# Optimization experiments

Measured on AMD Instinct MI355X. Metric: run time of the kernel, lower is better.

## Reference

```python
import jax, jax.numpy as jnp
import numpy as np
import math

B, N, D, L = 2, 256, 128, 4
TD = D // 2  # time embed dim
GROUPS = 32

def _interleave_sincos(v):
    # torch: stack((v[...,0::2].sin(), v[...,1::2].cos()), -1).flatten(last two)
    s = jnp.sin(v[..., 0::2])
    c = jnp.cos(v[..., 1::2])
    return jnp.stack([s, c], axis=-1).reshape(v.shape[:-1] + (-1,))

def _pos_embed(coords):
    # PositionEmbeddingSine(num_pos_feats=D//2, normalize=True, scale=2*pi)
    npf = D // 2
    dim_t = jnp.power(10000.0, 2.0 * jnp.floor(jnp.arange(npf, dtype=jnp.float32) / 2.0) / npf)
    scale = 2.0 * math.pi
    py = _interleave_sincos((coords[:, :, 0] * scale)[:, :, None] / dim_t)
    px = _interleave_sincos((coords[:, :, 1] * scale)[:, :, None] / dim_t)
    return jnp.concatenate([py, px], axis=-1)  # (B,N,D)

def _edge_pos_embed(adj):
    # ScalarEmbeddingSine(num_pos_feats=D, normalize=False)
    dim_t = jnp.power(10000.0, 2.0 * jnp.floor(jnp.arange(D, dtype=jnp.float32) / 2.0) / D)
    return _interleave_sincos(adj[:, :, :, None] / dim_t)  # (B,N,N,D)

def _timestep_embedding(t, dim):
    half = dim // 2
    freqs = jnp.exp(-math.log(10000.0) * jnp.arange(half, dtype=jnp.float32) / half)
    args = t.astype(jnp.float32)[:, None] * freqs
    return jnp.concatenate([jnp.cos(args), jnp.sin(args)], axis=-1)  # (B,D)

def _ln(x, s, b, eps=1e-5):
    mu = jnp.mean(x, -1, keepdims=True)
    var = jnp.var(x, -1, keepdims=True)
    return (x - mu) * jax.lax.rsqrt(var + eps) * s + b

def _gn(x, s, b, groups=GROUPS, eps=1e-5):
    # GroupNorm32 over (B, C, H, W)
    bb, c, h, w = x.shape
    xg = x.reshape(bb, groups, c // groups, h, w)
    mu = jnp.mean(xg, (2, 3, 4), keepdims=True)
    var = jnp.var(xg, (2, 3, 4), keepdims=True)
    xg = (xg - mu) * jax.lax.rsqrt(var + eps)
    return xg.reshape(bb, c, h, w) * s[None, :, None, None] + b[None, :, None, None]

def _forward(coords, adj_t, t, node_W, node_b, edge_W, edge_b, te1_W, te1_b, te2_W, te2_b,
             A_W, A_b, B_W, B_b, C_W, C_b, U_W, U_b, V_W, V_b,
             lnh_s, lnh_b, lne_s, lne_b, tl_W, tl_b,
             plo_ln_s, plo_ln_b, plo_W, plo_b, gn_s, gn_b, conv_W, conv_b):
    x = _pos_embed(coords) @ node_W + node_b            # (B,N,D)
    e = _edge_pos_embed(adj_t) @ edge_W + edge_b        # (B,N,N,D)
    te = _timestep_embedding(t, D) @ te1_W + te1_b
    te = jax.nn.relu(te) @ te2_W + te2_b                # (B,TD)
    for i in range(L):
        x_in, e_in = x, e
        # GatedGCNLayer (mode=direct, no internal residual)
        Uh = x @ U_W[i] + U_b[i]
        Vh = x @ V_W[i] + V_b[i]
        gate_input = ((x @ A_W[i] + A_b[i])[:, :, None, :]
                      + (x @ B_W[i] + B_b[i])[:, None, :, :]
                      + (e @ C_W[i] + C_b[i]))          # (B,N,N,D)
        gates = jax.nn.sigmoid(gate_input)
        agg = jnp.einsum('bijd,bjd->bid', gates, Vh)     # sum over neighbors j
        h_new = jax.nn.relu(_ln(Uh + agg, lnh_s[i], lnh_b[i]))
        e_new = jax.nn.relu(_ln(gate_input, lne_s[i], lne_b[i]))
        # time injection into edges: ReLU -> Linear(TD->D)
        e_new = e_new + (jax.nn.relu(te) @ tl_W[i] + tl_b[i])[:, None, None, :]
        # external residuals + per-layer out (LN -> SiLU -> Linear)
        x = x_in + h_new
        e = e_in + jax.nn.silu(_ln(e_new, plo_ln_s[i], plo_ln_b[i])) @ plo_W[i] + plo_b[i]
    eo = jnp.transpose(e, (0, 3, 1, 2))                  # (B,D,N,N)
    eo = jax.nn.relu(_gn(eo, gn_s, gn_b))
    out = jnp.einsum('bdij,do->boij', eo, conv_W) + conv_b[None, :, None, None]
    return out                                           # (B,1,N,N)

def setup_inputs() -> dict:
    key = jax.random.key(0)
    ks = iter(jax.random.split(key, 64))
    def w(shape, scale=0.02):
        return jax.random.normal(next(ks), shape, dtype=jnp.float32) * scale
    f32 = jnp.float32
    return {
        'coords': jax.random.uniform(next(ks), (B, N, 2), dtype=f32),
        'adj_t': jax.random.normal(next(ks), (B, N, N), dtype=f32),
        't': jax.random.uniform(next(ks), (B,), dtype=f32) * 1000.0,
        'node_W': w((D, D)), 'node_b': jnp.zeros((D,), f32),
        'edge_W': w((D, D)), 'edge_b': jnp.zeros((D,), f32),
        'te1_W': w((D, TD)), 'te1_b': jnp.zeros((TD,), f32),
        'te2_W': w((TD, TD)), 'te2_b': jnp.zeros((TD,), f32),
        'A_W': w((L, D, D)), 'A_b': jnp.zeros((L, D), f32),
        'B_W': w((L, D, D)), 'B_b': jnp.zeros((L, D), f32),
        'C_W': w((L, D, D)), 'C_b': jnp.zeros((L, D), f32),
        'U_W': w((L, D, D)), 'U_b': jnp.zeros((L, D), f32),
        'V_W': w((L, D, D)), 'V_b': jnp.zeros((L, D), f32),
        'lnh_s': jnp.ones((L, D), f32), 'lnh_b': jnp.zeros((L, D), f32),
        'lne_s': jnp.ones((L, D), f32), 'lne_b': jnp.zeros((L, D), f32),
        'tl_W': w((L, TD, D)), 'tl_b': jnp.zeros((L, D), f32),
        'plo_ln_s': jnp.ones((L, D), f32), 'plo_ln_b': jnp.zeros((L, D), f32),
        'plo_W': w((L, D, D)), 'plo_b': jnp.zeros((L, D), f32),
        'gn_s': jnp.ones((D,), f32), 'gn_b': jnp.zeros((D,), f32),
        'conv_W': w((D, 1)), 'conv_b': jnp.zeros((1,), f32),
    }

def reference(coords, adj_t, t, node_W, node_b, edge_W, edge_b, te1_W, te1_b, te2_W, te2_b,
              A_W, A_b, B_W, B_b, C_W, C_b, U_W, U_b, V_W, V_b,
              lnh_s, lnh_b, lne_s, lne_b, tl_W, tl_b,
              plo_ln_s, plo_ln_b, plo_W, plo_b, gn_s, gn_b, conv_W, conv_b):
    return _forward(coords, adj_t, t, node_W, node_b, edge_W, edge_b, te1_W, te1_b, te2_W, te2_b,
                    A_W, A_b, B_W, B_b, C_W, C_b, U_W, U_b, V_W, V_b,
                    lnh_s, lnh_b, lne_s, lne_b, tl_W, tl_b,
                    plo_ln_s, plo_ln_b, plo_W, plo_b, gn_s, gn_b, conv_W, conv_b)
```

## Files before the change

### kernel.cpp

```cpp
#include <hip/hip_runtime.h>
#include <hip/hip_bf16.h>

typedef unsigned short u16;
typedef __attribute__((ext_vector_type(8))) short short8;
typedef __attribute__((ext_vector_type(8))) unsigned short ushort8;
typedef __attribute__((ext_vector_type(4))) float f32x4;

#define BB 2
#define NN 256
#define DD 128
#define TDD 64
#define LL 4
#define NGROUP 32
#define NROWS (BB*NN*NN)
#define LDS_STR 68

#define LOG1E4 9.210340371976184f
#define TWO_PI 6.283185307179586f

#define TILE_GEMM(AT, WPTR, ACC) do {                                          \
  _Pragma("unroll 4")                                                          \
  for (int k = 0; k < 128; ++k) {                                              \
    const float4 w4 = *reinterpret_cast<const float4*>((WPTR) + k*128 + tx*4); \
    const float4 a0 = *reinterpret_cast<const float4*>(&(AT)[k*LDS_STR + ty*8]);     \
    const float4 a1 = *reinterpret_cast<const float4*>(&(AT)[k*LDS_STR + ty*8 + 4]); \
    const float av[8] = {a0.x,a0.y,a0.z,a0.w,a1.x,a1.y,a1.z,a1.w};             \
    const float wv[4] = {w4.x,w4.y,w4.z,w4.w};                                 \
    _Pragma("unroll") for (int r = 0; r < 8; ++r)                              \
      _Pragma("unroll") for (int c = 0; c < 4; ++c)                            \
        ACC[r][c] += av[r]*wv[c];                                              \
  }                                                                            \
} while (0)

__device__ __forceinline__ float sigmoidf_(float x) {
  return 1.f / (1.f + __expf(-x));
}

__device__ __forceinline__ u16 f2bf(float f) {
  union { float f; unsigned int u; } c; c.f = f;
  unsigned int r = (c.u + 0x7FFFu + ((c.u >> 16) & 1u)) >> 16;
  return (u16)r;
}

__global__ __launch_bounds__(512) void k_time(
    const float* __restrict__ t,
    const float* __restrict__ te1_W, const float* __restrict__ te1_b,
    const float* __restrict__ te2_W, const float* __restrict__ te2_b,
    const float* __restrict__ tl_W,  const float* __restrict__ tl_b,
    float* __restrict__ tproj) {
  __shared__ float temb[BB][128], h1[BB][64], rt[BB][64];
  const int tid = threadIdx.x;
  const int b  = tid >> 8;
  const int t2 = tid & 255;
  const float tv = t[b];
  if (t2 < 128) {
    int j = t2 & 63;
    float f = expf(-LOG1E4 * (float)j / 64.f);
    float a = tv * f;
    temb[b][t2] = (t2 < 64) ? cosf(a) : sinf(a);
  }
  __syncthreads();
  if (t2 < 64) {
    float acc = te1_b[t2];
#pragma unroll
    for (int k = 0; k < 128; ++k) acc += temb[b][k] * te1_W[k*64 + t2];
    h1[b][t2] = fmaxf(acc, 0.f);
  }
  __syncthreads();
  if (t2 < 64) {
    float acc = te2_b[t2];
#pragma unroll
    for (int k = 0; k < 64; ++k) acc += h1[b][k] * te2_W[k*64 + t2];
    rt[b][t2] = fmaxf(acc, 0.f);
  }
  __syncthreads();
  if (t2 < 128) {
#pragma unroll
    for (int i = 0; i < LL; ++i) {
      float acc = tl_b[i*128 + t2];
#pragma unroll
      for (int k = 0; k < 64; ++k) acc += rt[b][k] * tl_W[(i*64 + k)*128 + t2];
      tproj[(i*BB + b)*128 + t2] = acc;
    }
  }
}

__global__ __launch_bounds__(256) void k_node_embed(
    const float* __restrict__ coords, const float* __restrict__ W,
    const float* __restrict__ bias, float* __restrict__ x_out) {
  __shared__ float at[128*LDS_STR];
  int tid = threadIdx.x;
  int row = tid >> 2, part = tid & 3;
  int R = blockIdx.x*64 + row;
  float cy = coords[R*2 + 0], cx = coords[R*2 + 1];
#pragma unroll
  for (int q = 0; q < 32; ++q) {
    int c = part*32 + q;
    int k = (c < 64) ? c : c - 64;
    float v = (c < 64) ? cy : cx;
    int m = k >> 1;
    float inv = __expf(-LOG1E4 * (float)m / 32.f);
    float a = v * TWO_PI * inv;
    at[c*LDS_STR + row] = (k & 1) ? __cosf(a) : __sinf(a);
  }
  __syncthreads();
  int tx = tid & 31, ty = tid >> 5;
  float acc[8][4] = {};
  TILE_GEMM(at, W, acc);
  float4 bb4 = *reinterpret_cast<const float4*>(bias + tx*4);
#pragma unroll
  for (int r = 0; r < 8; ++r) {
    int R2 = blockIdx.x*64 + ty*8 + r;
    float4 o = {acc[r][0]+bb4.x, acc[r][1]+bb4.y, acc[r][2]+bb4.z, acc[r][3]+bb4.w};
    *reinterpret_cast<float4*>(x_out + (size_t)R2*128 + tx*4) = o;
  }
}

__global__ __launch_bounds__(256) void k_wprep_e(
    const float* __restrict__ EW, u16* __restrict__ WTE) {
  int idx = blockIdx.x*256 + threadIdx.x;
  int n = idx >> 7, k = idx & 127;
  WTE[n*128 + k] = f2bf(EW[(size_t)k*128 + n]);
}

__global__ __launch_bounds__(256, 3) void k_edge_embed2(
    const float* __restrict__ adj, const u16* __restrict__ WTE,
    const float* __restrict__ bias, float* __restrict__ e_out) {
  __shared__ __align__(16) u16 Abuf[64*128];
  __shared__ __align__(16) u16 Wbuf[128*128];

  const int tid = threadIdx.x;
  const int blk = blockIdx.x;
  const int w  = tid >> 6;
  const int l  = tid & 63;
  const int lg = l >> 4;
  const int ln = l & 15;

  {
    const int r = tid >> 1, h = tid & 1;
    const int r7 = r & 7;
    const u16* src = WTE + r*128;
    u16* dst = Wbuf + r*128;
#pragma unroll
    for (int q = 0; q < 8; ++q) {
      int c = h*8 + q;
      short8 v = *reinterpret_cast<const short8*>(src + c*8);
      *reinterpret_cast<short8*>(dst + ((c ^ r7) << 3)) = v;
    }
  }
  {
    const int r = tid >> 2;
    const int p = tid & 3;
    const float v = adj[(size_t)blk*64 + r];
    const int r7 = r & 7;
    u16* arow = Abuf + r*128;
#pragma unroll
    for (int q = 0; q < 4; ++q) {
      u16 h8[8];
#pragma unroll
      for (int j = 0; j < 8; ++j) {
        int k = (p*4 + q)*8 + j;
        int m = k >> 1;
        float inv = __expf(-LOG1E4 * (float)m / 64.f);
        float a = v * inv;
        h8[j] = f2bf((k & 1) ? __cosf(a) : __sinf(a));
      }
      int pc = (p*4 + q) ^ r7;
      *reinterpret_cast<ushort8*>(arow + pc*8) = *reinterpret_cast<ushort8*>(h8);
    }
  }
  __syncthreads();

  f32x4 acc[8];
#pragma unroll
  for (int nt = 0; nt < 8; ++nt) {
    const float bv = bias[nt*16 + ln];
#pragma unroll
    for (int rg = 0; rg < 4; ++rg) acc[nt][rg] = bv;
  }
  {
    const u16* arow = Abuf + (w*16 + ln)*128;
    const int r7 = ln & 7;
#pragma unroll
    for (int ks = 0; ks < 4; ++ks) {
      short8 a = *reinterpret_cast<const short8*>(arow + (((ks*4 + lg) ^ r7) << 3));
#pragma unroll
      for (int nt = 0; nt < 8; ++nt) {
        short8 bw = *reinterpret_cast<const short8*>(
            Wbuf + (nt*16 + ln)*128 + (((ks*4 + lg) ^ (ln & 7)) << 3));
        acc[nt] = __builtin_amdgcn_mfma_f32_16x16x32_bf16(a, bw, acc[nt], 0, 0, 0);
      }
    }
  }
#pragma unroll
  for (int nt = 0; nt < 8; ++nt)
#pragma unroll
    for (int rg = 0; rg < 4; ++rg)
      e_out[((size_t)blk*64 + w*16 + lg*4 + rg)*128 + nt*16 + ln] = acc[nt][rg];
}

__global__ __launch_bounds__(128) void k_node4(
    const float* __restrict__ x,
    const float* __restrict__ UW, const float* __restrict__ Ub,
    const float* __restrict__ VW, const float* __restrict__ Vb,
    const float* __restrict__ AW, const float* __restrict__ Ab,
    const float* __restrict__ BW, const float* __restrict__ Bb,
    float* __restrict__ Uh, float* __restrict__ Vh,
    float* __restrict__ Axo, float* __restrict__ Bxo) {
  __shared__ float xr[128];
  int R = blockIdx.x, d = threadIdx.x;
  xr[d] = x[(size_t)R*128 + d];
  __syncthreads();
  float au = Ub[d], av = Vb[d], aa = Ab[d], ab = Bb[d];
  for (int k = 0; k < 128; ++k) {
    float xv = xr[k];
    au += xv * UW[k*128 + d];
    av += xv * VW[k*128 + d];
    aa += xv * AW[k*128 + d];
    ab += xv * BW[k*128 + d];
  }
  Uh[(size_t)R*128 + d] = au;
  Vh[(size_t)R*128 + d] = av;
  Axo[(size_t)R*128 + d] = aa;
  Bxo[(size_t)R*128 + d] = ab;
}

__global__ __launch_bounds__(128) void k_xnode(
    const float* __restrict__ aggP,
    const float* __restrict__ lnh_s, const float* __restrict__ lnh_b,
    float* __restrict__ x,
    const float* __restrict__ UW, const float* __restrict__ Ub,
    const float* __restrict__ VW, const float* __restrict__ Vb,
    const float* __restrict__ AW, const float* __restrict__ Ab,
    const float* __restrict__ BW, const float* __restrict__ Bb,
    float* __restrict__ Uh, float* __restrict__ Vh,
    float* __restrict__ Axo, float* __restrict__ Bxo) {
  __shared__ float xr[128];
  __shared__ float red[4];
  int bi = blockIdx.x, d = threadIdx.x;
  float u = Uh[(size_t)bi*128 + d];
#pragma unroll
  for (int st = 0; st < 16; ++st) u += aggP[((size_t)bi*16 + st)*128 + d];
  float s = u, s2 = u*u;
#pragma unroll
  for (int m = 1; m <= 32; m <<= 1) { s += __shfl_xor(s, m); s2 += __shfl_xor(s2, m); }
  int wid = d >> 6;
  if ((d & 63) == 0) { red[wid] = s; red[2 + wid] = s2; }
  __syncthreads();
  s = red[0] + red[1];  s2 = red[2] + red[3];
  float mean = s * (1.f/128.f);
  float rs = rsqrtf(s2 * (1.f/128.f) - mean*mean + 1e-5f);
  float xv = x[(size_t)bi*128 + d] + fmaxf((u - mean)*rs*lnh_s[d] + lnh_b[d], 0.f);
  x[(size_t)bi*128 + d] = xv;
  xr[d] = xv;
  __syncthreads();
  float au = Ub[d], av = Vb[d], aa = Ab[d], ab = Bb[d];
  for (int k = 0; k < 128; ++k) {
    float xk = xr[k];
    au += xk * UW[k*128 + d];
    av += xk * VW[k*128 + d];
    aa += xk * AW[k*128 + d];
    ab += xk * BW[k*128 + d];
  }
  Uh[(size_t)bi*128 + d] = au;
  Vh[(size_t)bi*128 + d] = av;
  Axo[(size_t)bi*128 + d] = aa;
  Bxo[(size_t)bi*128 + d] = ab;
}

__global__ __launch_bounds__(256) void k_wprep(
    const float* __restrict__ CW, const float* __restrict__ PW,
    u16* __restrict__ WTC, u16* __restrict__ WTP) {
  int idx = blockIdx.x*256 + threadIdx.x;
  int m = idx >> 14;
  int r = idx & 16383;
  int layer = m >> 1;
  int n = r >> 7, k = r & 127;
  if ((m & 1) == 0)
    WTC[layer*16384 + n*128 + k] = f2bf(CW[(size_t)layer*16384 + k*128 + n]);
  else
    WTP[layer*16384 + n*128 + k] = f2bf(PW[(size_t)layer*16384 + k*128 + n]);
}

__global__ __launch_bounds__(512, 2) void k_layer(
    float* __restrict__ e,
    const u16* __restrict__ WTC, const u16* __restrict__ WTP,
    const float* __restrict__ Cb, const float* __restrict__ Ax,
    const float* __restrict__ Bx, const float* __restrict__ Vh,
    const float* __restrict__ lnes_g, const float* __restrict__ lneb_g,
    const float* __restrict__ tp_g,
    const float* __restrict__ plos_g, const float* __restrict__ plobl_g,
    const float* __restrict__ plob_g,
    float* __restrict__ aggP) {

  __shared__ __align__(16) u16 Abuf[128*128];
  __shared__ __align__(16) u16 Wbuf[128*128];

  const int tid = threadIdx.x;
  const int blk0 = blockIdx.x;
  const int blk = ((blk0 & 7) << 7) | (blk0 >> 3);
  const int bi  = blk >> 1;
  const int b   = bi >> 8;
  const int jh  = blk & 1;
  const size_t rbase = (size_t)bi*256 + jh*128;

  const int w  = tid >> 6;
  const int l  = tid & 63;
  const int lg = l >> 4;
  const int ln = l & 15;

  {
    const int r = tid >> 2;
    const int p = tid & 3;
    const float* src = e + (rbase + r)*128 + p*32;
    const int r7 = r & 7;
    u16* arow = Abuf + r*128;
#pragma unroll
    for (int q = 0; q < 4; ++q) {
      float4 f0 = *reinterpret_cast<const float4*>(src + q*8);
      float4 f1 = *reinterpret_cast<const float4*>(src + q*8 + 4);
      int pc = (p*4 + q) ^ r7;
      ushort8 h = {f2bf(f0.x),f2bf(f0.y),f2bf(f0.z),f2bf(f0.w),
                   f2bf(f1.x),f2bf(f1.y),f2bf(f1.z),f2bf(f1.w)};
      *reinterpret_cast<ushort8*>(arow + pc*8) = h;
    }
  }
  {
    const int r = tid >> 2;
    const int h = tid & 3;
    const int r7 = r & 7;
    const u16* src = WTC + r*128;
    u16* dst = Wbuf + r*128;
#pragma unroll
    for (int q = 0; q < 4; ++q) {
      int c = h*4 + q;
      short8 v = *reinterpret_cast<const short8*>(src + c*8);
      *reinterpret_cast<short8*>(dst + ((c ^ r7) << 3)) = v;
    }
  }
  __syncthreads();

  const int lrow0 = w*16 + lg*4;
  const int jrow0 = jh*128 + lrow0;

  f32x4 acc[8];
#pragma unroll
  for (int nt = 0; nt < 8; ++nt) {
    const int c = nt*16 + ln;
    const float cbax = Cb[c] + Ax[(size_t)bi*128 + c];
#pragma unroll
    for (int rg = 0; rg < 4; ++rg)
      acc[nt][rg] = cbax + Bx[((size_t)b*256 + jrow0 + rg)*128 + c];
  }

  {
    const u16* arow = Abuf + (w*16 + ln)*128;
    const int r7 = ln & 7;
#pragma unroll
    for (int ks = 0; ks < 4; ++ks) {
      short8 a = *reinterpret_cast<const short8*>(arow + (((ks*4 + lg) ^ r7) << 3));
#pragma unroll
      for (int nt = 0; nt < 8; ++nt) {
        short8 bw = *reinterpret_cast<const short8*>(
            Wbuf + (nt*16 + ln)*128 + (((ks*4 + lg) ^ (ln & 7)) << 3));
        acc[nt] = __builtin_amdgcn_mfma_f32_16x16x32_bf16(a, bw, acc[nt], 0, 0, 0);
      }
    }
  }

  float av[8] = {0.f,0.f,0.f,0.f,0.f,0.f,0.f,0.f};
  float tp_[8], ls_[8], lb_[8], ps_[8], pl_[8];
#pragma unroll
  for (int nt = 0; nt < 8; ++nt) {
    const int c = nt*16 + ln;
    tp_[nt] = tp_g[b*128 + c];
    ls_[nt] = lnes_g[c];  lb_[nt] = lneb_g[c];
    ps_[nt] = plos_g[c];  pl_[nt] = plobl_g[c];
  }

#pragma unroll
  for (int rg = 0; rg < 4; ++rg) {
    float ss = 0.f, s2 = 0.f;
#pragma unroll
    for (int nt = 0; nt < 8; ++nt) { float g = acc[nt][rg]; ss += g; s2 += g*g; }
    ss += __shfl_xor(ss, 1);  s2 += __shfl_xor(s2, 1);
    ss += __shfl_xor(ss, 2);  s2 += __shfl_xor(s2, 2);
    ss += __shfl_xor(ss, 4);  s2 += __shfl_xor(s2, 4);
    ss += __shfl_xor(ss, 8);  s2 += __shfl_xor(s2, 8);
    const float mean = ss * (1.f/128.f);
    const float rs = rsqrtf(s2 * (1.f/128.f) - mean*mean + 1e-5f);
    const size_t vrow = ((size_t)b*256 + jrow0 + rg)*128;
    float s3 = 0.f, s4 = 0.f;
#pragma unroll
    for (int nt = 0; nt < 8; ++nt) {
      const float g = acc[nt][rg];
      av[nt] += Vh[vrow + nt*16 + ln] * sigmoidf_(g);
      float tv = fmaxf((g - mean)*rs*ls_[nt] + lb_[nt], 0.f) + tp_[nt];
      acc[nt][rg] = tv;
      s3 += tv;  s4 += tv*tv;
    }
    s3 += __shfl_xor(s3, 1);  s4 += __shfl_xor(s4, 1);
    s3 += __shfl_xor(s3, 2);  s4 += __shfl_xor(s4, 2);
    s3 += __shfl_xor(s3, 4);  s4 += __shfl_xor(s4, 4);
    s3 += __shfl_xor(s3, 8);  s4 += __shfl_xor(s4, 8);
    const float mean2 = s3 * (1.f/128.f);
    const float rs2 = rsqrtf(s4 * (1.f/128.f) - mean2*mean2 + 1e-5f);
    const int rr = lrow0 + rg;
    const int rr7 = rr & 7;
#pragma unroll
    for (int nt = 0; nt < 8; ++nt) {
      float vv = (acc[nt][rg] - mean2)*rs2*ps_[nt] + pl_[nt];
      vv = vv * sigmoidf_(vv);
      const int cc = nt*16 + ln;
      const int pc = (cc >> 3) ^ rr7;
      Abuf[rr*128 + pc*8 + (cc & 7)] = f2bf(vv);
    }
  }

  __syncthreads();
  {
    const int r = tid >> 2;
    const int h = tid & 3;
    const int r7 = r & 7;
    const u16* src = WTP + r*128;
    u16* dst = Wbuf + r*128;
#pragma unroll
    for (int q = 0; q < 4; ++q) {
      int c = h*4 + q;
      short8 v = *reinterpret_cast<const short8*>(src + c*8);
      *reinterpret_cast<short8*>(dst + ((c ^ r7) << 3)) = v;
    }
  }
  __syncthreads();

  f32x4 acc2[8];
#pragma unroll
  for (int nt = 0; nt < 8; ++nt) acc2[nt] = (f32x4)(0.f);
  {
    const u16* arow = Abuf + (w*16 + ln)*128;
    const int r7 = ln & 7;
#pragma unroll
    for (int ks = 0; ks < 4; ++ks) {
      short8 a = *reinterpret_cast<const short8*>(arow + (((ks*4 + lg) ^ r7) << 3));
#pragma unroll
      for (int nt = 0; nt < 8; ++nt) {
        short8 bw = *reinterpret_cast<const short8*>(
            Wbuf + (nt*16 + ln)*128 + (((ks*4 + lg) ^ (ln & 7)) << 3));
        acc2[nt] = __builtin_amdgcn_mfma_f32_16x16x32_bf16(a, bw, acc2[nt], 0, 0, 0);
      }
    }
  }

#pragma unroll
  for (int nt = 0; nt < 8; ++nt) {
    const float pbv = plob_g[nt*16 + ln];
#pragma unroll
    for (int rg = 0; rg < 4; ++rg) {
      float* ep = e + (rbase + lrow0 + rg)*128 + nt*16 + ln;
      *ep = *ep + acc2[nt][rg] + pbv;
    }
  }

#pragma unroll
  for (int nt = 0; nt < 8; ++nt) {
    float v = av[nt];
    v += __shfl_xor(v, 16);
    v += __shfl_xor(v, 32);
    av[nt] = v;
  }
  if (lg == 0) {
#pragma unroll
    for (int nt = 0; nt < 8; ++nt)
      aggP[((size_t)blk*8 + w)*128 + nt*16 + ln] = av[nt];
  }
}

__global__ __launch_bounds__(128) void k_xupd(
    const float* __restrict__ aggP, const float* __restrict__ Uh,
    const float* __restrict__ lnh_s, const float* __restrict__ lnh_b,
    float* __restrict__ x) {
  int bi = blockIdx.x, d = threadIdx.x;
  float u = Uh[(size_t)bi*128 + d];
#pragma unroll
  for (int st = 0; st < 16; ++st) u += aggP[((size_t)bi*16 + st)*128 + d];
  float s = u, s2 = u*u;
#pragma unroll
  for (int m = 1; m <= 32; m <<= 1) { s += __shfl_xor(s, m); s2 += __shfl_xor(s2, m); }
  __shared__ float red[4];
  int wid = d >> 6;
  if ((d & 63) == 0) { red[wid] = s; red[2 + wid] = s2; }
  __syncthreads();
  s = red[0] + red[1];  s2 = red[2] + red[3];
  float mean = s * (1.f/128.f);
  float rs = rsqrtf(s2 * (1.f/128.f) - mean*mean + 1e-5f);
  x[(size_t)bi*128 + d] += fmaxf((u - mean)*rs*lnh_s[d] + lnh_b[d], 0.f);
}

__global__ __launch_bounds__(128) void k_zero(float* __restrict__ p) {
  p[threadIdx.x] = 0.f;
}

__global__ __launch_bounds__(256) void k_gnstats2(
    const float* __restrict__ e, float* __restrict__ sraw) {
  const int blk = blockIdx.x;
  const int b = blk >> 8;
  const int c = threadIdx.x & 31;
  const int r0 = threadIdx.x >> 5;
  float s = 0.f, s2 = 0.f;
  for (int it = 0; it < 32; ++it) {
    size_t row = (size_t)blk*256 + it*8 + r0;
    float4 f = *reinterpret_cast<const float4*>(e + row*128 + c*4);
    s  += f.x + f.y + f.z + f.w;
    s2 += f.x*f.x + f.y*f.y + f.z*f.z + f.w*f.w;
  }
  __shared__ float red[256], red2[256];
  red[threadIdx.x] = s;  red2[threadIdx.x] = s2;
  __syncthreads();
  if (threadIdx.x < 32) {
    float S = 0.f, S2 = 0.f;
#pragma unroll
    for (int k = 0; k < 8; ++k) { S += red[k*32 + threadIdx.x]; S2 += red2[k*32 + threadIdx.x]; }
    atomicAdd(&sraw[((size_t)b*32 + threadIdx.x)*2],     S);
    atomicAdd(&sraw[((size_t)b*32 + threadIdx.x)*2 + 1], S2);
  }
}

__global__ __launch_bounds__(64) void k_gnfin(
    const float* __restrict__ raw, float* __restrict__ stats) {
  int i = threadIdx.x;
  const float cnt = (float)(NN*NN*4);
  float S  = raw[i*2];
  float S2 = raw[i*2 + 1];
  float mean = S / cnt;
  float var = S2 / cnt - mean*mean;
  stats[i*2]     = mean;
  stats[i*2 + 1] = rsqrtf(var + 1e-5f);
}

__global__ __launch_bounds__(256) void k_out(
    const float* __restrict__ e, const float* __restrict__ stats,
    const float* __restrict__ gn_s, const float* __restrict__ gn_b,
    const float* __restrict__ convW, const float* __restrict__ convb,
    float* __restrict__ out) {
  int tid = threadIdx.x;
  int row = tid >> 2, part = tid & 3;
  size_t R = (size_t)blockIdx.x*64 + row;
  size_t b = R >> 16;
  float acc = 0.f;
  const float4* er = reinterpret_cast<const float4*>(e + R*128 + part*32);
#pragma unroll
  for (int q = 0; q < 8; ++q) {
    float4 f = er[q];
    float fv[4] = {f.x, f.y, f.z, f.w};
#pragma unroll
    for (int lidx = 0; lidx < 4; ++lidx) {
      int c = part*32 + q*4 + lidx;
      int g = c >> 2;
      float mean = stats[(b*NGROUP + g)*2 + 0];
      float rs   = stats[(b*NGROUP + g)*2 + 1];
      float t = (fv[lidx] - mean)*rs*gn_s[c] + gn_b[c];
      acc += fmaxf(t, 0.f) * convW[c];
    }
  }
  acc += __shfl_xor(acc, 1);
  acc += __shfl_xor(acc, 2);
  if (part == 0) out[R] = acc + convb[0];
}

extern "C" void kernel_launch(void* const* d_in, const int* in_sizes, int n_in,
                              void* d_out, int out_size, void* d_ws, size_t ws_size,
                              hipStream_t stream) {
  const float* coords  = (const float*)d_in[0];
  const float* adj_t   = (const float*)d_in[1];
  const float* t       = (const float*)d_in[2];
  const float* node_W  = (const float*)d_in[3];
  const float* node_b  = (const float*)d_in[4];
  const float* edge_W  = (const float*)d_in[5];
  const float* edge_b  = (const float*)d_in[6];
  const float* te1_W   = (const float*)d_in[7];
  const float* te1_b   = (const float*)d_in[8];
  const float* te2_W   = (const float*)d_in[9];
  const float* te2_b   = (const float*)d_in[10];
  const float* A_W     = (const float*)d_in[11];
  const float* A_b     = (const float*)d_in[12];
  const float* B_W     = (const float*)d_in[13];
  const float* B_b     = (const float*)d_in[14];
  const float* C_W     = (const float*)d_in[15];
  const float* C_b     = (const float*)d_in[16];
  const float* U_W     = (const float*)d_in[17];
  const float* U_b     = (const float*)d_in[18];
  const float* V_W     = (const float*)d_in[19];
  const float* V_b     = (const float*)d_in[20];
  const float* lnh_s   = (const float*)d_in[21];
  const float* lnh_b   = (const float*)d_in[22];
  const float* lne_s   = (const float*)d_in[23];
  const float* lne_b   = (const float*)d_in[24];
  const float* tl_W    = (const float*)d_in[25];
  const float* tl_b    = (const float*)d_in[26];
  const float* plo_ln_s= (const float*)d_in[27];
  const float* plo_ln_b= (const float*)d_in[28];
  const float* plo_W   = (const float*)d_in[29];
  const float* plo_b   = (const float*)d_in[30];
  const float* gn_s    = (const float*)d_in[31];
  const float* gn_b    = (const float*)d_in[32];
  const float* conv_W  = (const float*)d_in[33];
  const float* conv_b  = (const float*)d_in[34];

  float* ws    = (float*)d_ws;
  float* e     = ws;
  float* x     = e + (size_t)NROWS*128;
  float* Uh    = x + 65536;
  float* Vh    = Uh + 65536;
  float* Ax    = Vh + 65536;
  float* Bx    = Ax + 65536;
  float* tproj = Bx + 65536;
  float* sraw  = tproj + 1024;
  float* stats = sraw + 128;
  float* aggP  = stats + 128;
  u16*   WTC   = (u16*)(aggP + 1048576);
  u16*   WTP   = WTC + (size_t)LL*16384;
  u16*   WTE   = WTP + (size_t)LL*16384;

  k_zero<<<1, 128, 0, stream>>>(sraw);
  k_wprep<<<512, 256, 0, stream>>>(C_W, plo_W, WTC, WTP);
  k_wprep_e<<<64, 256, 0, stream>>>(edge_W, WTE);
  k_time<<<1, 512, 0, stream>>>(t, te1_W, te1_b, te2_W, te2_b, tl_W, tl_b, tproj);
  k_node_embed<<<8, 256, 0, stream>>>(coords, node_W, node_b, x);
  k_edge_embed2<<<NROWS/64, 256, 0, stream>>>(adj_t, WTE, edge_b, e);

  for (int i = 0; i < LL; ++i) {
    if (i == 0) {
      k_node4<<<BB*NN, 128, 0, stream>>>(x,
          U_W, U_b, V_W, V_b, A_W, A_b, B_W, B_b,
          Uh, Vh, Ax, Bx);
    } else {
      k_xnode<<<BB*NN, 128, 0, stream>>>(aggP,
          lnh_s + (i-1)*128, lnh_b + (i-1)*128, x,
          U_W + (size_t)i*16384, U_b + i*128,
          V_W + (size_t)i*16384, V_b + i*128,
          A_W + (size_t)i*16384, A_b + i*128,
          B_W + (size_t)i*16384, B_b + i*128,
          Uh, Vh, Ax, Bx);
    }
    k_layer<<<NROWS/128, 512, 0, stream>>>(e,
        WTC + (size_t)i*16384, WTP + (size_t)i*16384,
        C_b + i*128, Ax, Bx, Vh,
        lne_s + i*128, lne_b + i*128,
        tproj + i*BB*128,
        plo_ln_s + i*128, plo_ln_b + i*128, plo_b + i*128,
        aggP);
  }
  k_xupd<<<BB*NN, 128, 0, stream>>>(aggP, Uh, lnh_s + 3*128, lnh_b + 3*128, x);

  k_gnstats2<<<512, 256, 0, stream>>>(e, sraw);
  k_gnfin<<<1, 64, 0, stream>>>(sraw, stats);
  k_out<<<NROWS/64, 256, 0, stream>>>(e, stats, gn_s, gn_b, conv_W, conv_b,
                                      (float*)d_out);
}
```

Before: 411.2 us.

## Fuse GroupNorm statistics into last edge layer and finalize stats in output kernel

Adds a variant of the edge layer kernel, used for the last layer only, that accumulates per-group sum and sum-of-squares of the updated edge features into shared memory and then atomically into a global buffer. This removes a separate full pass over the edge tensor (k_gnstats2) and the k_gnfin launch. k_out now computes mean and rstd per block from the raw sums into shared memory. The fused kernel adds shared and global atomics and extra register pressure in the last layer.

```diff
diff --git a/kernel.cpp b/kernel.cpp
--- a/kernel.cpp
+++ b/kernel.cpp
@@ -475,6 +475,222 @@
   }
 }
 
+__global__ __launch_bounds__(512, 2) void k_layer_s(
+    float* __restrict__ e,
+    const u16* __restrict__ WTC, const u16* __restrict__ WTP,
+    const float* __restrict__ Cb, const float* __restrict__ Ax,
+    const float* __restrict__ Bx, const float* __restrict__ Vh,
+    const float* __restrict__ lnes_g, const float* __restrict__ lneb_g,
+    const float* __restrict__ tp_g,
+    const float* __restrict__ plos_g, const float* __restrict__ plobl_g,
+    const float* __restrict__ plob_g,
+    float* __restrict__ aggP, float* __restrict__ sraw) {
+
+  __shared__ __align__(16) u16 Abuf[128*128];
+  __shared__ __align__(16) u16 Wbuf[128*128];
+  __shared__ float sgrp[64];
+
+  const int tid = threadIdx.x;
+  const int blk0 = blockIdx.x;
+  const int blk = ((blk0 & 7) << 7) | (blk0 >> 3);
+  const int bi  = blk >> 1;
+  const int b   = bi >> 8;
+  const int jh  = blk & 1;
+  const size_t rbase = (size_t)bi*256 + jh*128;
+
+  const int w  = tid >> 6;
+  const int l  = tid & 63;
+  const int lg = l >> 4;
+  const int ln = l & 15;
+
+  {
+    const int r = tid >> 2;
+    const int p = tid & 3;
+    const float* src = e + (rbase + r)*128 + p*32;
+    const int r7 = r & 7;
+    u16* arow = Abuf + r*128;
+#pragma unroll
+    for (int q = 0; q < 4; ++q) {
+      float4 f0 = *reinterpret_cast<const float4*>(src + q*8);
+      float4 f1 = *reinterpret_cast<const float4*>(src + q*8 + 4);
+      int pc = (p*4 + q) ^ r7;
+      ushort8 h = {f2bf(f0.x),f2bf(f0.y),f2bf(f0.z),f2bf(f0.w),
+                   f2bf(f1.x),f2bf(f1.y),f2bf(f1.z),f2bf(f1.w)};
+      *reinterpret_cast<ushort8*>(arow + pc*8) = h;
+    }
+  }
+  {
+    const int r = tid >> 2;
+    const int h = tid & 3;
+    const int r7 = r & 7;
+    const u16* src = WTC + r*128;
+    u16* dst = Wbuf + r*128;
+#pragma unroll
+    for (int q = 0; q < 4; ++q) {
+      int c = h*4 + q;
+      short8 v = *reinterpret_cast<const short8*>(src + c*8);
+      *reinterpret_cast<short8*>(dst + ((c ^ r7) << 3)) = v;
+    }
+  }
+  if (tid < 64) sgrp[tid] = 0.f;
+  __syncthreads();
+
+  const int lrow0 = w*16 + lg*4;
+  const int jrow0 = jh*128 + lrow0;
+
+  f32x4 acc[8];
+#pragma unroll
+  for (int nt = 0; nt < 8; ++nt) {
+    const int c = nt*16 + ln;
+    const float cbax = Cb[c] + Ax[(size_t)bi*128 + c];
+#pragma unroll
+    for (int rg = 0; rg < 4; ++rg)
+      acc[nt][rg] = cbax + Bx[((size_t)b*256 + jrow0 + rg)*128 + c];
+  }
+
+  {
+    const u16* arow = Abuf + (w*16 + ln)*128;
+    const int r7 = ln & 7;
+#pragma unroll
+    for (int ks = 0; ks < 4; ++ks) {
+      short8 a = *reinterpret_cast<const short8*>(arow + (((ks*4 + lg) ^ r7) << 3));
+#pragma unroll
+      for (int nt = 0; nt < 8; ++nt) {
+        short8 bw = *reinterpret_cast<const short8*>(
+            Wbuf + (nt*16 + ln)*128 + (((ks*4 + lg) ^ (ln & 7)) << 3));
+        acc[nt] = __builtin_amdgcn_mfma_f32_16x16x32_bf16(a, bw, acc[nt], 0, 0, 0);
+      }
+    }
+  }
+
+  float av[8] = {0.f,0.f,0.f,0.f,0.f,0.f,0.f,0.f};
+  float tp_[8], ls_[8], lb_[8], ps_[8], pl_[8];
+#pragma unroll
+  for (int nt = 0; nt < 8; ++nt) {
+    const int c = nt*16 + ln;
+    tp_[nt] = tp_g[b*128 + c];
+    ls_[nt] = lnes_g[c];  lb_[nt] = lneb_g[c];
+    ps_[nt] = plos_g[c];  pl_[nt] = plobl_g[c];
+  }
+
+#pragma unroll
+  for (int rg = 0; rg < 4; ++rg) {
+    float ss = 0.f, s2 = 0.f;
+#pragma unroll
+    for (int nt = 0; nt < 8; ++nt) { float g = acc[nt][rg]; ss += g; s2 += g*g; }
+    ss += __shfl_xor(ss, 1);  s2 += __shfl_xor(s2, 1);
+    ss += __shfl_xor(ss, 2);  s2 += __shfl_xor(s2, 2);
+    ss += __shfl_xor(ss, 4);  s2 += __shfl_xor(s2, 4);
+    ss += __shfl_xor(ss, 8);  s2 += __shfl_xor(s2, 8);
+    const float mean = ss * (1.f/128.f);
+    const float rs = rsqrtf(s2 * (1.f/128.f) - mean*mean + 1e-5f);
+    const size_t vrow = ((size_t)b*256 + jrow0 + rg)*128;
+    float s3 = 0.f, s4 = 0.f;
+#pragma unroll
+    for (int nt = 0; nt < 8; ++nt) {
+      const float g = acc[nt][rg];
+      av[nt] += Vh[vrow + nt*16 + ln] * sigmoidf_(g);
+      float tv = fmaxf((g - mean)*rs*ls_[nt] + lb_[nt], 0.f) + tp_[nt];
+      acc[nt][rg] = tv;
+      s3 += tv;  s4 += tv*tv;
+    }
+    s3 += __shfl_xor(s3, 1);  s4 += __shfl_xor(s4, 1);
+    s3 += __shfl_xor(s3, 2);  s4 += __shfl_xor(s4, 2);
+    s3 += __shfl_xor(s3, 4);  s4 += __shfl_xor(s4, 4);
+    s3 += __shfl_xor(s3, 8);  s4 += __shfl_xor(s4, 8);
+    const float mean2 = s3 * (1.f/128.f);
+    const float rs2 = rsqrtf(s4 * (1.f/128.f) - mean2*mean2 + 1e-5f);
+    const int rr = lrow0 + rg;
+    const int rr7 = rr & 7;
+#pragma unroll
+    for (int nt = 0; nt < 8; ++nt) {
+      float vv = (acc[nt][rg] - mean2)*rs2*ps_[nt] + pl_[nt];
+      vv = vv * sigmoidf_(vv);
+      const int cc = nt*16 + ln;
+      const int pc = (cc >> 3) ^ rr7;
+      Abuf[rr*128 + pc*8 + (cc & 7)] = f2bf(vv);
+    }
+  }
+
+  __syncthreads();
+  {
+    const int r = tid >> 2;
+    const int h = tid & 3;
+    const int r7 = r & 7;
+    const u16* src = WTP + r*128;
+    u16* dst = Wbuf + r*128;
+#pragma unroll
+    for (int q = 0; q < 4; ++q) {
+      int c = h*4 + q;
+      short8 v = *reinterpret_cast<const short8*>(src + c*8);
+      *reinterpret_cast<short8*>(dst + ((c ^ r7) << 3)) = v;
+    }
+  }
+  __syncthreads();
+
+  f32x4 acc2[8];
+#pragma unroll
+  for (int nt = 0; nt < 8; ++nt) acc2[nt] = (f32x4)(0.f);
+  {
+    const u16* arow = Abuf + (w*16 + ln)*128;
+    const int r7 = ln & 7;
+#pragma unroll
+    for (int ks = 0; ks < 4; ++ks) {
+      short8 a = *reinterpret_cast<const short8*>(arow + (((ks*4 + lg) ^ r7) << 3));
+#pragma unroll
+      for (int nt = 0; nt < 8; ++nt) {
+        short8 bw = *reinterpret_cast<const short8*>(
+            Wbuf + (nt*16 + ln)*128 + (((ks*4 + lg) ^ (ln & 7)) << 3));
+        acc2[nt] = __builtin_amdgcn_mfma_f32_16x16x32_bf16(a, bw, acc2[nt], 0, 0, 0);
+      }
+    }
+  }
+
+#pragma unroll
+  for (int nt = 0; nt < 8; ++nt) {
+    const float pbv = plob_g[nt*16 + ln];
+#pragma unroll
+    for (int rg = 0; rg < 4; ++rg) {
+      float* ep = e + (rbase + lrow0 + rg)*128 + nt*16 + ln;
+      float v = *ep + acc2[nt][rg] + pbv;
+      *ep = v;
+      acc2[nt][rg] = v;
+    }
+  }
+
+#pragma unroll
+  for (int nt = 0; nt < 8; ++nt) {
+    float gs = acc2[nt][0] + acc2[nt][1] + acc2[nt][2] + acc2[nt][3];
+    float gq = acc2[nt][0]*acc2[nt][0] + acc2[nt][1]*acc2[nt][1]
+             + acc2[nt][2]*acc2[nt][2] + acc2[nt][3]*acc2[nt][3];
+    gs += __shfl_xor(gs, 1);  gq += __shfl_xor(gq, 1);
+    gs += __shfl_xor(gs, 2);  gq += __shfl_xor(gq, 2);
+    gs += __shfl_xor(gs, 16); gq += __shfl_xor(gq, 16);
+    gs += __shfl_xor(gs, 32); gq += __shfl_xor(gq, 32);
+    if ((l & 51) == 0) {
+      int g = nt*4 + (ln >> 2);
+      atomicAdd(&sgrp[g*2],     gs);
+      atomicAdd(&sgrp[g*2 + 1], gq);
+    }
+  }
+  __syncthreads();
+  if (tid < 64)
+    atomicAdd(&sraw[(size_t)b*64 + tid], sgrp[tid]);
+
+#pragma unroll
+  for (int nt = 0; nt < 8; ++nt) {
+    float v = av[nt];
+    v += __shfl_xor(v, 16);
+    v += __shfl_xor(v, 32);
+    av[nt] = v;
+  }
+  if (lg == 0) {
+#pragma unroll
+    for (int nt = 0; nt < 8; ++nt)
+      aggP[((size_t)blk*8 + w)*128 + nt*16 + ln] = av[nt];
+  }
+}
+
 __global__ __launch_bounds__(128) void k_xupd(
     const float* __restrict__ aggP, const float* __restrict__ Uh,
     const float* __restrict__ lnh_s, const float* __restrict__ lnh_b,
@@ -500,52 +716,26 @@
   p[threadIdx.x] = 0.f;
 }
 
-__global__ __launch_bounds__(256) void k_gnstats2(
-    const float* __restrict__ e, float* __restrict__ sraw) {
-  const int blk = blockIdx.x;
-  const int b = blk >> 8;
-  const int c = threadIdx.x & 31;
-  const int r0 = threadIdx.x >> 5;
-  float s = 0.f, s2 = 0.f;
-  for (int it = 0; it < 32; ++it) {
-    size_t row = (size_t)blk*256 + it*8 + r0;
-    float4 f = *reinterpret_cast<const float4*>(e + row*128 + c*4);
-    s  += f.x + f.y + f.z + f.w;
-    s2 += f.x*f.x + f.y*f.y + f.z*f.z + f.w*f.w;
-  }
-  __shared__ float red[256], red2[256];
-  red[threadIdx.x] = s;  red2[threadIdx.x] = s2;
-  __syncthreads();
-  if (threadIdx.x < 32) {
-    float S = 0.f, S2 = 0.f;
-#pragma unroll
-    for (int k = 0; k < 8; ++k) { S += red[k*32 + threadIdx.x]; S2 += red2[k*32 + threadIdx.x]; }
-    atomicAdd(&sraw[((size_t)b*32 + threadIdx.x)*2],     S);
-    atomicAdd(&sraw[((size_t)b*32 + threadIdx.x)*2 + 1], S2);
-  }
-}
-
-__global__ __launch_bounds__(64) void k_gnfin(
-    const float* __restrict__ raw, float* __restrict__ stats) {
-  int i = threadIdx.x;
-  const float cnt = (float)(NN*NN*4);
-  float S  = raw[i*2];
-  float S2 = raw[i*2 + 1];
-  float mean = S / cnt;
-  float var = S2 / cnt - mean*mean;
-  stats[i*2]     = mean;
-  stats[i*2 + 1] = rsqrtf(var + 1e-5f);
-}
-
 __global__ __launch_bounds__(256) void k_out(
-    const float* __restrict__ e, const float* __restrict__ stats,
+    const float* __restrict__ e, const float* __restrict__ sraw,
     const float* __restrict__ gn_s, const float* __restrict__ gn_b,
     const float* __restrict__ convW, const float* __restrict__ convb,
     float* __restrict__ out) {
+  __shared__ float st[64];
   int tid = threadIdx.x;
+  size_t b = ((size_t)blockIdx.x*64) >> 16;
+  if (tid < 32) {
+    const float cnt = (float)(NN*NN*4);
+    float S  = sraw[b*64 + tid*2];
+    float S2 = sraw[b*64 + tid*2 + 1];
+    float mean = S / cnt;
+    float var = S2 / cnt - mean*mean;
+    st[tid*2]     = mean;
+    st[tid*2 + 1] = rsqrtf(var + 1e-5f);
+  }
+  __syncthreads();
   int row = tid >> 2, part = tid & 3;
   size_t R = (size_t)blockIdx.x*64 + row;
-  size_t b = R >> 16;
   float acc = 0.f;
   const float4* er = reinterpret_cast<const float4*>(e + R*128 + part*32);
 #pragma unroll
@@ -556,8 +746,8 @@
     for (int lidx = 0; lidx < 4; ++lidx) {
       int c = part*32 + q*4 + lidx;
       int g = c >> 2;
-      float mean = stats[(b*NGROUP + g)*2 + 0];
-      float rs   = stats[(b*NGROUP + g)*2 + 1];
+      float mean = st[g*2 + 0];
+      float rs   = st[g*2 + 1];
       float t = (fv[lidx] - mean)*rs*gn_s[c] + gn_b[c];
       acc += fmaxf(t, 0.f) * convW[c];
     }
@@ -615,8 +805,7 @@
   float* Bx    = Ax + 65536;
   float* tproj = Bx + 65536;
   float* sraw  = tproj + 1024;
-  float* stats = sraw + 128;
-  float* aggP  = stats + 128;
+  float* aggP  = sraw + 128;
   u16*   WTC   = (u16*)(aggP + 1048576);
   u16*   WTP   = WTC + (size_t)LL*16384;
   u16*   WTE   = WTP + (size_t)LL*16384;
@@ -642,18 +831,26 @@
           B_W + (size_t)i*16384, B_b + i*128,
           Uh, Vh, Ax, Bx);
     }
-    k_layer<<<NROWS/128, 512, 0, stream>>>(e,
-        WTC + (size_t)i*16384, WTP + (size_t)i*16384,
-        C_b + i*128, Ax, Bx, Vh,
-        lne_s + i*128, lne_b + i*128,
-        tproj + i*BB*128,
-        plo_ln_s + i*128, plo_ln_b + i*128, plo_b + i*128,
-        aggP);
+    if (i < LL-1) {
+      k_layer<<<NROWS/128, 512, 0, stream>>>(e,
+          WTC + (size_t)i*16384, WTP + (size_t)i*16384,
+          C_b + i*128, Ax, Bx, Vh,
+          lne_s + i*128, lne_b + i*128,
+          tproj + i*BB*128,
+          plo_ln_s + i*128, plo_ln_b + i*128, plo_b + i*128,
+          aggP);
+    } else {
+      k_layer_s<<<NROWS/128, 512, 0, stream>>>(e,
+          WTC + (size_t)i*16384, WTP + (size_t)i*16384,
+          C_b + i*128, Ax, Bx, Vh,
+          lne_s + i*128, lne_b + i*128,
+          tproj + i*BB*128,
+          plo_ln_s + i*128, plo_ln_b + i*128, plo_b + i*128,
+          aggP, sraw);
+    }
   }
   k_xupd<<<BB*NN, 128, 0, stream>>>(aggP, Uh, lnh_s + 3*128, lnh_b + 3*128, x);
 
-  k_gnstats2<<<512, 256, 0, stream>>>(e, sraw);
-  k_gnfin<<<1, 64, 0, stream>>>(sraw, stats);
-  k_out<<<NROWS/64, 256, 0, stream>>>(e, stats, gn_s, gn_b, conv_W, conv_b,
+  k_out<<<NROWS/64, 256, 0, stream>>>(e, sraw, gn_s, gn_b, conv_W, conv_b,
                                       (float*)d_out);
 }
```

After: 396.5 us. 3.6% less time.
